# Performance work log

Measured on AMD Instinct MI355X. Metric: run time of the kernel, lower is better.

## Reference

```python
import jax, jax.numpy as jnp
import numpy as np

T, B, H, L, V = 256, 64, 1024, 2, 32000
Hh = H // 2
MAX_FORGET = 0.875  # forget gate z in (1-max_forget, 1)


def setup_inputs() -> dict:
    key = jax.random.key(0)
    ks = jax.random.split(key, 12)
    s = 0.02
    def w(k, shape):
        return (jax.random.normal(k, shape, jnp.float32) * s)
    return {
        "input_seq": jax.random.randint(ks[0], (T, B), 0, V),
        "h0": jax.random.normal(ks[1], (L, B, H), jnp.float32),
        "emb": w(ks[2], (V, H)),
        "W_zr1": w(ks[3], (L, H + Hh, H)),   "b_zr1": jnp.zeros((L, H), jnp.float32),
        "W_g1":  w(ks[4], (L, H + Hh, Hh)), "b_g1":  jnp.zeros((L, Hh), jnp.float32),
        "W_zr2": w(ks[5], (L, H + Hh, H)),   "b_zr2": jnp.zeros((L, H), jnp.float32),
        "W_g2":  w(ks[6], (L, H + Hh, Hh)), "b_g2":  jnp.zeros((L, Hh), jnp.float32),
    }


def _revgru_cell(x, h, Wzr1, bzr1, Wg1, bg1, Wzr2, bzr2, Wg2, bg2):
    # x: [B,H], h: [B,H] split into two halves that update each other (reversible GRU)
    h1, h2 = h[:, :Hh], h[:, Hh:]
    zr1 = jnp.concatenate([x, h2], axis=1) @ Wzr1 + bzr1
    z1 = jax.nn.sigmoid(zr1[:, :Hh]) * MAX_FORGET + (1.0 - MAX_FORGET)
    r1 = jax.nn.sigmoid(zr1[:, Hh:])
    g1 = jnp.tanh(jnp.concatenate([x, r1 * h2], axis=1) @ Wg1 + bg1)
    h1n = z1 * h1 + (1.0 - z1) * g1
    zr2 = jnp.concatenate([x, h1n], axis=1) @ Wzr2 + bzr2
    z2 = jax.nn.sigmoid(zr2[:, :Hh]) * MAX_FORGET + (1.0 - MAX_FORGET)
    r2 = jax.nn.sigmoid(zr2[:, Hh:])
    g2 = jnp.tanh(jnp.concatenate([x, r2 * h1n], axis=1) @ Wg2 + bg2)
    h2n = z2 * h2 + (1.0 - z2) * g2
    return jnp.concatenate([h1n, h2n], axis=1)


def reference(input_seq, h0, emb, W_zr1, b_zr1, W_g1, b_g1, W_zr2, b_zr2, W_g2, b_g2):
    # Dropout rates are 0 (module defaults), so all locked-dropout layers are identity.
    x_seq = emb[input_seq]  # [T,B,H]

    def step(hiddens, x_t):  # hiddens: [L,B,H]
        cur = x_t
        new = []
        for l in range(L):
            hn = _revgru_cell(cur, hiddens[l], W_zr1[l], b_zr1[l], W_g1[l], b_g1[l],
                              W_zr2[l], b_zr2[l], W_g2[l], b_g2[l])
            new.append(hn)
            cur = hn  # output_hidden feeds next layer (lockdroph is identity)
        return jnp.stack(new), None

    final, _ = jax.lax.scan(step, h0, x_seq)
    return final  # [L,B,H] last hidden per layer
```

## Files before the change

kernel.cpp:

```cpp
#include <hip/hip_runtime.h>

#define T_   256
#define B_   64
#define H_   1024
#define Hh_  512
#define L_   2
#define K1_  1536
#define MAXF 0.875f
#define NBLK 128
#define NT   1024

#define OFF_WZR1 0u
#define OFF_WG1  3145728u
#define OFF_WZR2 4718592u
#define OFF_WG2  7864320u
#define OFF_XT   9437184u
#define OFF_HT   9568256u
#define OFF_ZT   9830400u
#define OFF_RHT  9895936u
#define OFF_CTR  9961472u

__global__ __launch_bounds__(256) void retile_w(const float* __restrict__ src,
                                                float* __restrict__ dst,
                                                int N, int C) {
    size_t tid = (size_t)blockIdx.x * 256 + threadIdx.x;
    size_t total = (size_t)L_ * K1_ * N;
    if (tid >= total) return;
    int c = (int)(tid % C);
    int k = (int)((tid / C) % K1_);
    int b = (int)((tid / ((size_t)C * K1_)) % (N / C));
    int l = (int)(tid / ((size_t)C * K1_ * (N / C)));
    dst[tid] = src[((size_t)l * K1_ + k) * N + b * C + c];
}

__device__ __forceinline__ float ld_coh(const float* p) {
    return __hip_atomic_load(p, __ATOMIC_RELAXED, __HIP_MEMORY_SCOPE_AGENT);
}
__device__ __forceinline__ void st_coh(float* p, float v) {
    __hip_atomic_store(p, v, __ATOMIC_RELAXED, __HIP_MEMORY_SCOPE_AGENT);
}

__device__ __forceinline__ void gbar(unsigned* ctr, unsigned* target) {
    *target += NBLK;
    __syncthreads();
    if (threadIdx.x == 0) {
        __hip_atomic_fetch_add(ctr, 1u, __ATOMIC_RELAXED, __HIP_MEMORY_SCOPE_AGENT);
        while (__hip_atomic_load(ctr, __ATOMIC_RELAXED, __HIP_MEMORY_SCOPE_AGENT) < *target)
            __builtin_amdgcn_s_sleep(1);
    }
    __syncthreads();
}

template<int C>
__device__ __forceinline__ float phase_gemm(const float* __restrict__ Axlo,
                                            const float* __restrict__ Ahi,
                                            const float* __restrict__ Wt,
                                            float* __restrict__ red) {
    const int tid  = threadIdx.x;
    const int lane = tid & 63;
    const int w    = __builtin_amdgcn_readfirstlane(tid >> 6);
    const int k0   = w * 96;
    for (int i = tid; i < 64 * (C + 1); i += NT) red[i] = 0.f;
    float acc[C];
#pragma unroll
    for (int c = 0; c < C; ++c) acc[c] = 0.f;
    __syncthreads();
#pragma unroll 1
    for (int kb = 0; kb < 96; kb += 8) {
        float av[8];
#pragma unroll
        for (int j = 0; j < 8; ++j) {
            const int k = k0 + kb + j;
            const float* ap = (k < H_) ? (Axlo + (size_t)k * 64)
                                       : (Ahi + (size_t)(k - H_) * 64);
            av[j] = ld_coh(ap + lane);
        }
#pragma unroll
        for (int j = 0; j < 8; ++j) {
            const float* wr = Wt + (size_t)(k0 + kb + j) * C;
#pragma unroll
            for (int c = 0; c < C; ++c) acc[c] = fmaf(av[j], wr[c], acc[c]);
        }
    }
#pragma unroll
    for (int c = 0; c < C; ++c) atomicAdd(&red[lane * (C + 1) + c], acc[c]);
    __syncthreads();
    float v = 0.f;
    if (tid < 64 * C) v = red[(tid / C) * (C + 1) + (tid % C)];
    return v;
}

__global__ __launch_bounds__(NT) void revgru_main(
    const int* __restrict__ seq, const float* __restrict__ h0,
    const float* __restrict__ emb,
    const float* __restrict__ bzr1, const float* __restrict__ bg1,
    const float* __restrict__ bzr2, const float* __restrict__ bg2,
    float* __restrict__ ws, float* __restrict__ out)
{
    const int bi = blockIdx.x, tid = threadIdx.x;
    const int l = (bi >= 64) ? 1 : 0, bl = bi & 63;
    __shared__ float red[64 * 17];
    unsigned target = 0;

    float* xT  = ws + OFF_XT;
    float* hT  = ws + OFF_HT;
    float* zT  = ws + OFF_ZT;
    float* rhT = ws + OFF_RHT;
    unsigned* ctr = (unsigned*)(ws + OFF_CTR);

    const float* Wz1  = ws + OFF_WZR1 + ((size_t)l * 64 + bl) * K1_ * 16;
    const float* Wg1l = ws + OFF_WG1  + ((size_t)l * 64 + bl) * K1_ * 8;
    const float* Wz2  = ws + OFF_WZR2 + ((size_t)l * 64 + bl) * K1_ * 16;
    const float* Wg2l = ws + OFF_WG2  + ((size_t)l * 64 + bl) * K1_ * 8;

    const int gtid = bi * NT + tid;
    {
        int ll = gtid >> 16, rem = gtid & 65535, r = rem >> 10, n = rem & 1023;
        st_coh(&hT[(((size_t)ll * 2 + 1) * H_ + n) * 64 + r], h0[gtid]);
        if (bi < 64) {
            int k = gtid >> 6, rr = gtid & 63;
            st_coh(&xT[gtid], emb[(size_t)seq[rr] * H_ + k]);
        }
    }
    gbar(ctr, &target);

    for (int s = 0; s <= T_; ++s) {
        const int t = (l == 0) ? s : s - 1;
        const bool act = (t >= 0) && (t < T_);
        const int buf = t & 1;
        float* hC = hT + ((size_t)l * 2 + buf) * (H_ * 64);
        float* hP = hT + ((size_t)l * 2 + (buf ^ 1)) * (H_ * 64);
        const float* Ax = (l == 0) ? (xT + (size_t)buf * (H_ * 64))
                                   : (hT + (size_t)buf * (H_ * 64));
        float* zl  = zT  + (size_t)l * Hh_ * 64;
        float* rhl = rhT + (size_t)l * Hh_ * 64;

        if (act) {
            float v = phase_gemm<16>(Ax, hP + Hh_ * 64, Wz1, red);
            int r = tid >> 4, c = tid & 15, n = bl * 16 + c;
            v += bzr1[l * H_ + n];
            float sg = 1.f / (1.f + __expf(-v));
            if (n < Hh_) st_coh(&zl[n * 64 + r], sg * MAXF + (1.f - MAXF));
            else st_coh(&rhl[(n - Hh_) * 64 + r],
                        sg * ld_coh(&hP[(size_t)n * 64 + r]));
            if (l == 0 && t + 1 < T_) {
                int k = gtid >> 6, rr = gtid & 63;
                st_coh(&xT[(size_t)((t + 1) & 1) * (H_ * 64) + k * 64 + rr],
                       emb[(size_t)seq[(t + 1) * B_ + rr] * H_ + k]);
            }
        }
        gbar(ctr, &target);
        if (act) {
            float v = phase_gemm<8>(Ax, rhl, Wg1l, red);
            if (tid < 512) {
                int r = tid >> 3, c = tid & 7, n = bl * 8 + c;
                float g = tanhf(v + bg1[l * Hh_ + n]);
                float z = ld_coh(&zl[n * 64 + r]);
                float h1o = ld_coh(&hP[(size_t)n * 64 + r]);
                st_coh(&hC[(size_t)n * 64 + r], z * h1o + (1.f - z) * g);
            }
        }
        gbar(ctr, &target);
        if (act) {
            float v = phase_gemm<16>(Ax, hC, Wz2, red);
            int r = tid >> 4, c = tid & 15, n = bl * 16 + c;
            v += bzr2[l * H_ + n];
            float sg = 1.f / (1.f + __expf(-v));
            if (n < Hh_) st_coh(&zl[n * 64 + r], sg * MAXF + (1.f - MAXF));
            else st_coh(&rhl[(n - Hh_) * 64 + r],
                        sg * ld_coh(&hC[(size_t)(n - Hh_) * 64 + r]));
        }
        gbar(ctr, &target);
        if (act) {
            float v = phase_gemm<8>(Ax, rhl, Wg2l, red);
            if (tid < 512) {
                int r = tid >> 3, c = tid & 7, n = bl * 8 + c;
                float g = tanhf(v + bg2[l * Hh_ + n]);
                float z = ld_coh(&zl[n * 64 + r]);
                float h2o = ld_coh(&hP[(size_t)(Hh_ + n) * 64 + r]);
                st_coh(&hC[(size_t)(Hh_ + n) * 64 + r], z * h2o + (1.f - z) * g);
            }
        }
        gbar(ctr, &target);
    }
    {
        int ll = gtid >> 16, rem = gtid & 65535, r = rem >> 10, n = rem & 1023;
        out[gtid] = ld_coh(&hT[(((size_t)ll * 2 + 1) * H_ + n) * 64 + r]);
    }
}

extern "C" void kernel_launch(void* const* d_in, const int* in_sizes, int n_in,
                              void* d_out, int out_size, void* d_ws, size_t ws_size,
                              hipStream_t stream) {
    (void)in_sizes; (void)n_in; (void)out_size; (void)ws_size;
    const int*   seq  = (const int*)  d_in[0];
    const float* h0   = (const float*)d_in[1];
    const float* emb  = (const float*)d_in[2];
    const float* Wzr1 = (const float*)d_in[3];
    const float* bzr1 = (const float*)d_in[4];
    const float* Wg1  = (const float*)d_in[5];
    const float* bg1  = (const float*)d_in[6];
    const float* Wzr2 = (const float*)d_in[7];
    const float* bzr2 = (const float*)d_in[8];
    const float* Wg2  = (const float*)d_in[9];
    const float* bg2  = (const float*)d_in[10];
    float* out = (float*)d_out;
    float* ws  = (float*)d_ws;

    hipMemsetAsync((char*)d_ws + (size_t)OFF_CTR * 4, 0, 64, stream);
    retile_w<<<12288, 256, 0, stream>>>(Wzr1, ws + OFF_WZR1, H_, 16);
    retile_w<<<6144,  256, 0, stream>>>(Wg1,  ws + OFF_WG1,  Hh_, 8);
    retile_w<<<12288, 256, 0, stream>>>(Wzr2, ws + OFF_WZR2, H_, 16);
    retile_w<<<6144,  256, 0, stream>>>(Wg2,  ws + OFF_WG2,  Hh_, 8);

    void* args[] = { &seq, &h0, &emb, &bzr1, &bg1, &bzr2, &bg2, &ws, &out };
    hipLaunchCooperativeKernel((void*)revgru_main, dim3(NBLK), dim3(NT),
                               args, 0, stream);
}
```

Before: 48.07 ms.

## Stage per-block weights through double-buffered LDS with activation prefetch

The per-phase GEMM now splits the K dimension into six 256-row chunks. Each chunk's weight slice is staged into a double-buffered LDS tile with float4 loads, and the next chunk's weights and activations are prefetched into registers while the current chunk is computed. Previously each warp streamed its own 96-row K slice of weights directly from global memory with uniform scalar loads. The aim is to hide global and L2 latency in the recurrent inner loop, at the cost of two block-wide syncs per chunk and extra LDS traffic.

```diff
diff --git a/kernel.cpp b/kernel.cpp
--- a/kernel.cpp
+++ b/kernel.cpp
@@ -55,32 +55,59 @@
 __device__ __forceinline__ float phase_gemm(const float* __restrict__ Axlo,
                                             const float* __restrict__ Ahi,
                                             const float* __restrict__ Wt,
+                                            float* __restrict__ ldsW,
                                             float* __restrict__ red) {
     const int tid  = threadIdx.x;
     const int lane = tid & 63;
-    const int w    = __builtin_amdgcn_readfirstlane(tid >> 6);
-    const int k0   = w * 96;
+    const int w    = tid >> 6;
+    constexpr int KCH = 256, NCH = K1_ / KCH;
+    constexpr int CHF = KCH * C;
+    constexpr int CHV = CHF / 4;
+    const int kw0 = w * 16;
+
     for (int i = tid; i < 64 * (C + 1); i += NT) red[i] = 0.f;
+
     float acc[C];
 #pragma unroll
     for (int c = 0; c < C; ++c) acc[c] = 0.f;
-    __syncthreads();
-#pragma unroll 1
-    for (int kb = 0; kb < 96; kb += 8) {
-        float av[8];
-#pragma unroll
-        for (int j = 0; j < 8; ++j) {
-            const int k = k0 + kb + j;
-            const float* ap = (k < H_) ? (Axlo + (size_t)k * 64)
-                                       : (Ahi + (size_t)(k - H_) * 64);
-            av[j] = ld_coh(ap + lane);
-        }
-#pragma unroll
-        for (int j = 0; j < 8; ++j) {
-            const float* wr = Wt + (size_t)(k0 + kb + j) * C;
-#pragma unroll
-            for (int c = 0; c < C; ++c) acc[c] = fmaf(av[j], wr[c], acc[c]);
-        }
+
+    float4* buf4 = (float4*)ldsW;
+    const float4* W4 = (const float4*)Wt;
+    float4 pref;
+    if (tid < CHV) pref = W4[tid];
+
+    float avc[16], avn[16];
+#pragma unroll
+    for (int kk = 0; kk < 16; ++kk)
+        avc[kk] = ld_coh(Axlo + (size_t)(kw0 + kk) * 64 + lane);
+
+    for (int j = 0; j < NCH; ++j) {
+        if (tid < CHV) buf4[(j & 1) * CHV + tid] = pref;
+        if (j + 1 < NCH) {
+            const int kb = (j + 1) * KCH;
+            const float* Ap = (kb < H_) ? (Axlo + (size_t)kb * 64)
+                                        : (Ahi + (size_t)(kb - H_) * 64);
+#pragma unroll
+            for (int kk = 0; kk < 16; ++kk)
+                avn[kk] = ld_coh(Ap + (size_t)(kw0 + kk) * 64 + lane);
+            if (tid < CHV) pref = W4[(size_t)(j + 1) * CHV + tid];
+        }
+        __syncthreads();
+        const float* lw = ldsW + (j & 1) * CHF + kw0 * C;
+#pragma unroll
+        for (int kk = 0; kk < 16; ++kk) {
+#pragma unroll
+            for (int c4 = 0; c4 < C / 4; ++c4) {
+                const float4 wv = *(const float4*)&lw[kk * C + c4 * 4];
+                acc[c4 * 4 + 0] = fmaf(avc[kk], wv.x, acc[c4 * 4 + 0]);
+                acc[c4 * 4 + 1] = fmaf(avc[kk], wv.y, acc[c4 * 4 + 1]);
+                acc[c4 * 4 + 2] = fmaf(avc[kk], wv.z, acc[c4 * 4 + 2]);
+                acc[c4 * 4 + 3] = fmaf(avc[kk], wv.w, acc[c4 * 4 + 3]);
+            }
+        }
+        __syncthreads();
+#pragma unroll
+        for (int kk = 0; kk < 16; ++kk) avc[kk] = avn[kk];
     }
 #pragma unroll
     for (int c = 0; c < C; ++c) atomicAdd(&red[lane * (C + 1) + c], acc[c]);
@@ -99,6 +126,7 @@
 {
     const int bi = blockIdx.x, tid = threadIdx.x;
     const int l = (bi >= 64) ? 1 : 0, bl = bi & 63;
+    __shared__ float ldsW[2 * 256 * 16];
     __shared__ float red[64 * 17];
     unsigned target = 0;
 
@@ -136,7 +164,7 @@
         float* rhl = rhT + (size_t)l * Hh_ * 64;
 
         if (act) {
-            float v = phase_gemm<16>(Ax, hP + Hh_ * 64, Wz1, red);
+            float v = phase_gemm<16>(Ax, hP + Hh_ * 64, Wz1, ldsW, red);
             int r = tid >> 4, c = tid & 15, n = bl * 16 + c;
             v += bzr1[l * H_ + n];
             float sg = 1.f / (1.f + __expf(-v));
@@ -151,7 +179,7 @@
         }
         gbar(ctr, &target);
         if (act) {
-            float v = phase_gemm<8>(Ax, rhl, Wg1l, red);
+            float v = phase_gemm<8>(Ax, rhl, Wg1l, ldsW, red);
             if (tid < 512) {
                 int r = tid >> 3, c = tid & 7, n = bl * 8 + c;
                 float g = tanhf(v + bg1[l * Hh_ + n]);
@@ -162,7 +190,7 @@
         }
         gbar(ctr, &target);
         if (act) {
-            float v = phase_gemm<16>(Ax, hC, Wz2, red);
+            float v = phase_gemm<16>(Ax, hC, Wz2, ldsW, red);
             int r = tid >> 4, c = tid & 15, n = bl * 16 + c;
             v += bzr2[l * H_ + n];
             float sg = 1.f / (1.f + __expf(-v));
@@ -172,7 +200,7 @@
         }
         gbar(ctr, &target);
         if (act) {
-            float v = phase_gemm<8>(Ax, rhl, Wg2l, red);
+            float v = phase_gemm<8>(Ax, rhl, Wg2l, ldsW, red);
             if (tid < 512) {
                 int r = tid >> 3, c = tid & 7, n = bl * 8 + c;
                 float g = tanhf(v + bg2[l * Hh_ + n]);
```

New measurement: 164.3 ms. 3.42x slower.
